# Optimization experiments

Hardware: AMD Instinct MI355X
Metric: run time of the kernel (lower is better)

The kernel has to match this reference:

```python
import jax, jax.numpy as jnp
import numpy as np
import math

B, S, D, H = 16, 1024, 768, 12
Dh = D // H  # 64


def setup_inputs() -> dict:
    key = jax.random.key(0)
    ks = jax.random.split(key, 9)
    scale = 1.0 / math.sqrt(D)
    X = jax.random.normal(ks[0], (B, S, D), dtype=jnp.float32)
    # Per-head Q/K/V projections stacked along head dim: [H, D, Dh]
    Wq = jax.random.normal(ks[1], (H, D, Dh), dtype=jnp.float32) * scale
    Wk = jax.random.normal(ks[2], (H, D, Dh), dtype=jnp.float32) * scale
    Wv = jax.random.normal(ks[3], (H, D, Dh), dtype=jnp.float32) * scale
    bq = jax.random.normal(ks[4], (H, Dh), dtype=jnp.float32) * scale
    bk = jax.random.normal(ks[5], (H, Dh), dtype=jnp.float32) * scale
    bv = jax.random.normal(ks[6], (H, Dh), dtype=jnp.float32) * scale
    Wo = jax.random.normal(ks[7], (D, D), dtype=jnp.float32) * scale
    bo = jax.random.normal(ks[8], (D,), dtype=jnp.float32) * scale
    return {"X": X, "Wq": Wq, "bq": bq, "Wk": Wk, "bk": bk,
            "Wv": Wv, "bv": bv, "Wo": Wo, "bo": bo}


def reference(X, Wq, bq, Wk, bk, Wv, bv, Wo, bo):
    # Batched multi-head QKV projections (equivalent to the per-head Linear loop).
    Q = jnp.einsum('bsd,hde->bhse', X, Wq) + bq[None, :, None, :]
    K = jnp.einsum('bsd,hde->bhse', X, Wk) + bk[None, :, None, :]
    V = jnp.einsum('bsd,hde->bhse', X, Wv) + bv[None, :, None, :]
    scores = jnp.einsum('bhse,bhte->bhst', Q, K) / jnp.sqrt(jnp.float32(Dh))
    A = jax.nn.softmax(scores, axis=-1)            # [B,H,S,S]
    O = jnp.einsum('bhst,bhte->bhse', A, V)        # [B,H,S,Dh]
    # Concat heads along feature dim (matches torch cat order: head 0 first).
    msa = jnp.transpose(O, (0, 2, 1, 3)).reshape(B, S, D)
    return msa @ Wo + bo
```

## Files before the change

### kernel.cpp

```cpp
#include <hip/hip_runtime.h>
#include <hip/hip_bf16.h>

#define BB 16
#define SS 1024
#define DD 768
#define HH 12
#define DH 64

typedef short short8 __attribute__((ext_vector_type(8)));
typedef float f32x4 __attribute__((ext_vector_type(4)));

__device__ inline float b2f(unsigned short v) {
    union { unsigned int u; float f; } x; x.u = ((unsigned int)v) << 16; return x.f;
}
__device__ inline unsigned short f2b(float f) {
    unsigned int u = __float_as_uint(f);
    u += 0x7FFFu + ((u >> 16) & 1u);
    return (unsigned short)(u >> 16);
}
__device__ inline unsigned int pk2(float a, float b) {
    __hip_bfloat162 h = __float22bfloat162_rn(make_float2(a, b));
    return *(unsigned int*)&h;
}
__device__ inline void cvt8(unsigned short* dst, const float* src) {
    const float4 f0 = *(const float4*)src;
    const float4 f1 = *(const float4*)(src + 4);
    unsigned short t[8] = {f2b(f0.x), f2b(f0.y), f2b(f0.z), f2b(f0.w),
                           f2b(f1.x), f2b(f1.y), f2b(f1.z), f2b(f1.w)};
    *(uint4*)dst = *(const uint4*)t;
}
__device__ __forceinline__ void async16(const void* g, void* l) {
    __builtin_amdgcn_global_load_lds(
        (const __attribute__((address_space(1))) void*)g,
        (__attribute__((address_space(3))) void*)l, 16, 0, 0);
}

__global__ __launch_bounds__(256) void detect_kernel(const unsigned short* __restrict__ X,
                                                     int* __restrict__ flag) {
    __shared__ int s;
    if (threadIdx.x == 0) s = 0;
    __syncthreads();
    int c = 0;
    for (int i = threadIdx.x; i < 16384; i += 256) {
        unsigned short v = X[i];
        if ((v & 0x7FFFu) >= 0x7F80u) c = 1;
    }
    if (c) s = 1;
    __syncthreads();
    if (threadIdx.x == 0) flag[0] = s;
}

__global__ __launch_bounds__(256) void prep_x(const void* __restrict__ Xv,
                                              const int* __restrict__ flag,
                                              unsigned short* __restrict__ Xb) {
    const int dt = *flag;
    size_t base = ((size_t)blockIdx.x * 256 + threadIdx.x) * 8;
    if (dt) cvt8(Xb + base, (const float*)Xv + base);
    else    *(uint4*)(Xb + base) = *(const uint4*)((const unsigned short*)Xv + base);
}

__global__ __launch_bounds__(256) void prep_w(
    const void* __restrict__ Wqv, const void* __restrict__ Wkv,
    const void* __restrict__ Wvv, const void* __restrict__ Wov,
    const int* __restrict__ flag,
    unsigned short* __restrict__ Wc, unsigned short* __restrict__ Wot)
{
    __shared__ unsigned short Ls[64][72];
    const int dt = *flag;
    const int u = threadIdx.x;
    const int kt = blockIdx.x;
    const int y  = blockIdx.y;
    const int rk = u >> 2;
    const int e0 = (u & 3) * 16;

    const void* src;
    size_t srcBase;
    unsigned short* dst; int drow;
    if (y < 36) {
        int z = y / 12, h = y % 12;
        src = (z == 0) ? Wqv : (z == 1) ? Wkv : Wvv;
        srcBase = ((size_t)h * DD + kt * 64 + rk) * DH;
        dst = Wc; drow = z * 768 + h * 64;
    } else {
        int nt = y - 36;
        src = Wov;
        srcBase = (size_t)(kt * 64 + rk) * DD + nt * 64;
        dst = Wot; drow = nt * 64;
    }

#pragma unroll
    for (int ii = 0; ii < 2; ++ii) {
        int e = e0 + ii * 8;
        if (dt) {
            const float* p = (const float*)src + srcBase + e;
            float4 a = *(const float4*)p, b = *(const float4*)(p + 4);
            float v[8] = {a.x, a.y, a.z, a.w, b.x, b.y, b.z, b.w};
#pragma unroll
            for (int j = 0; j < 8; ++j) Ls[e + j][rk] = f2b(v[j]);
        } else {
            union { uint4 v; unsigned short s[8]; } t;
            t.v = *(const uint4*)((const unsigned short*)src + srcBase + e);
#pragma unroll
            for (int j = 0; j < 8; ++j) Ls[e + j][rk] = t.s[j];
        }
    }
    __syncthreads();
    const int e = u >> 2, q = u & 3;
#pragma unroll
    for (int ii = 0; ii < 2; ++ii) {
        int kk = q * 16 + ii * 8;
        *(uint4*)(dst + (size_t)(drow + e) * DD + kt * 64 + kk) = *(const uint4*)(&Ls[e][kk]);
    }
}

__global__ __launch_bounds__(256) void prep_bias(
    const void* __restrict__ bqv, const void* __restrict__ bkv,
    const void* __restrict__ bvv, const void* __restrict__ bov,
    const int* __restrict__ flag,
    unsigned short* __restrict__ bc, float* __restrict__ bo32)
{
    const int dt = *flag;
    for (int n = threadIdx.x; n < 2304; n += 256) {
        int z = n / 768, i = n % 768;
        const void* b = (z == 0) ? bqv : (z == 1) ? bkv : bvv;
        bc[n] = dt ? f2b(((const float*)b)[i]) : ((const unsigned short*)b)[i];
    }
    for (int n = threadIdx.x; n < 768; n += 256)
        bo32[n] = dt ? ((const float*)bov)[n] : b2f(((const unsigned short*)bov)[n]);
}

__global__ __launch_bounds__(256) void qkv_gemm(
    const unsigned short* __restrict__ Xb,
    const unsigned short* __restrict__ Wc,
    const unsigned short* __restrict__ bc,
    unsigned short* __restrict__ Qb, unsigned short* __restrict__ Kb,
    unsigned short* __restrict__ Vtb)
{
    __shared__ __align__(16) unsigned short lds[17408];
    unsigned short* As = lds;
    unsigned short* Bs = lds + 128 * 64;

    const int u = threadIdx.x;
    const int lane = u & 63, w = u >> 6;
    const int ln = lane & 15, quad = lane >> 4;
    const int wm = w & 1, wn = w >> 1;

    const int nt0 = blockIdx.x;
    const int m0  = blockIdx.y << 7;
    const int n0  = nt0 << 7;
    const int z   = nt0 / 6;
    const int hpair = (nt0 % 6) * 2;

    const int rA = w * 32 + (lane >> 3);
    const int c8 = (((lane & 7) ^ (lane >> 3)) * 8);

    f32x4 acc[4][4];
#pragma unroll
    for (int i = 0; i < 4; ++i)
#pragma unroll
        for (int j = 0; j < 4; ++j) acc[i][j] = (f32x4){0.f, 0.f, 0.f, 0.f};

    const unsigned short* Ag = Xb + (size_t)(m0 + rA) * DD + c8;
    const unsigned short* Bg = Wc + (size_t)(n0 + rA) * DD + c8;
    unsigned short* lA0 = As + w * 2048;
    unsigned short* lB0 = Bs + w * 2048;

    for (int kb = 0; kb < 12; ++kb) {
        const int k0 = kb * 64;
        if (kb) __syncthreads();
#pragma unroll
        for (int j = 0; j < 4; ++j) {
            async16(Ag + (size_t)j * 8 * DD + k0, lA0 + j * 512);
            async16(Bg + (size_t)j * 8 * DD + k0, lB0 + j * 512);
        }
        __syncthreads();
#pragma unroll
        for (int kh = 0; kh < 2; ++kh) {
            const int sx = ((kh * 4 + quad) ^ (ln & 7)) * 8;
            short8 af[4], bf[4];
#pragma unroll
            for (int t = 0; t < 4; ++t) {
                af[t] = *(const short8*)(As + (wm * 64 + t * 16 + ln) * 64 + sx);
                bf[t] = *(const short8*)(Bs + (wn * 64 + t * 16 + ln) * 64 + sx);
            }
#pragma unroll
            for (int mt = 0; mt < 4; ++mt)
#pragma unroll
                for (int nt = 0; nt < 4; ++nt)
                    acc[mt][nt] = __builtin_amdgcn_mfma_f32_16x16x32_bf16(af[mt], bf[nt], acc[mt][nt], 0, 0, 0);
        }
    }

    float bias[4];
#pragma unroll
    for (int nt = 0; nt < 4; ++nt) bias[nt] = b2f(bc[n0 + wn * 64 + nt * 16 + ln]);

    const int b = m0 >> 10;
    if (z < 2) {
        unsigned short* O = (z == 0) ? Qb : Kb;
        const int h = hpair + wn;
        const int sb = (m0 & 1023) + wm * 64;
#pragma unroll
        for (int mt = 0; mt < 4; ++mt)
#pragma unroll
            for (int r = 0; r < 4; ++r) {
                int s = sb + mt * 16 + quad * 4 + r;
                size_t rowo = ((size_t)(b * HH + h) * SS + s) * DH;
#pragma unroll
                for (int nt = 0; nt < 4; ++nt)
                    O[rowo + nt * 16 + ln] = f2b(acc[mt][nt][r] + bias[nt]);
            }
    } else {
        __syncthreads();
#pragma unroll
        for (int mt = 0; mt < 4; ++mt)
#pragma unroll
            for (int nt = 0; nt < 4; ++nt)
#pragma unroll
                for (int r = 0; r < 4; ++r)
                    lds[(wn * 64 + nt * 16 + ln) * 136 + wm * 64 + mt * 16 + quad * 4 + r] =
                        f2b(acc[mt][nt][r] + bias[nt]);
        __syncthreads();
        const int cc = u >> 1, half = u & 1;
        const int h = hpair + (cc >> 6), e = cc & 63;
        const int sb = (m0 & 1023) + half * 64;
        unsigned short* dst = Vtb + ((size_t)(b * HH + h) * DH + e) * SS + sb;
        const unsigned short* srcp = lds + cc * 136 + half * 64;
#pragma unroll
        for (int i = 0; i < 8; ++i)
            *(uint4*)(dst + i * 8) = *(const uint4*)(srcp + i * 8);
    }
}

__global__ __launch_bounds__(256) void attn_kernel(
    const unsigned short* __restrict__ Kb,
    const unsigned short* __restrict__ Vtb,
    unsigned short* __restrict__ Qb)
{
    __shared__ __align__(16) unsigned short Qs[64][72];
    __shared__ __align__(16) unsigned short Ks[4096];
    __shared__ __align__(16) unsigned short Vs[4096];
    __shared__ __align__(16) unsigned short Ps[64][72];

    const int u = threadIdx.x;
    const int s0 = blockIdx.x << 6;
    const int bh = blockIdx.y;

    const int lane = u & 63, w = u >> 6;
    const int ln = lane & 15, quad = lane >> 4;

    unsigned short* Qg = Qb + ((size_t)bh * SS + s0) * DH;
    const unsigned short* Kg = Kb + (size_t)bh * SS * DH;
    const unsigned short* Vg = Vtb + (size_t)bh * DH * SS;

    const int xrow = u >> 3, xch = u & 7;
#pragma unroll
    for (int p = 0; p < 2; ++p) {
        int r2 = xrow + 32 * p;
        *(uint4*)(&Qs[r2][xch * 8]) = *(const uint4*)(Qg + r2 * DH + xch * 8);
    }
    __syncthreads();
    short8 qf0 = *(const short8*)(&Qs[16 * w + ln][quad * 8]);
    short8 qf1 = *(const short8*)(&Qs[16 * w + ln][32 + quad * 8]);

    short8 ones;
#pragma unroll
    for (int i = 0; i < 8; ++i) ones[i] = (short)0x3F80;

    f32x4 acc_o[4];
#pragma unroll
    for (int i = 0; i < 4; ++i) acc_o[i] = (f32x4){0.f, 0.f, 0.f, 0.f};
    f32x4 acc_l = (f32x4){0.f, 0.f, 0.f, 0.f};

    const float Csc = 0.125f * 1.44269504088896f;

    const int srow = (lane >> 3);
    const int cg8  = ((lane & 7) ^ srow) * 8;

    for (int kt = 0; kt < 16; ++kt) {
        const int t0 = kt << 6;
        __syncthreads();
#pragma unroll
        for (int j = 0; j < 2; ++j) {
            const int r0 = (w * 2 + j) * 8 + srow;
            async16(Kg + (size_t)(t0 + r0) * DH + cg8, Ks + (w * 2 + j) * 512);
            async16(Vg + (size_t)r0 * SS + t0 + cg8,  Vs + (w * 2 + j) * 512);
        }
        __syncthreads();

        f32x4 acc_s[4];
#pragma unroll
        for (int nt = 0; nt < 4; ++nt) {
            const int sx0 = (quad ^ (ln & 7)) * 8;
            const int sx1 = ((4 + quad) ^ (ln & 7)) * 8;
            short8 kf0 = *(const short8*)(Ks + (nt * 16 + ln) * 64 + sx0);
            short8 kf1 = *(const short8*)(Ks + (nt * 16 + ln) * 64 + sx1);
            f32x4 zz = (f32x4){0.f, 0.f, 0.f, 0.f};
            zz = __builtin_amdgcn_mfma_f32_16x16x32_bf16(kf0, qf0, zz, 0, 0, 0);
            zz = __builtin_amdgcn_mfma_f32_16x16x32_bf16(kf1, qf1, zz, 0, 0, 0);
            acc_s[nt] = zz;
        }

#pragma unroll
        for (int nt = 0; nt < 4; ++nt) {
            float p0 = exp2f(acc_s[nt][0] * Csc);
            float p1 = exp2f(acc_s[nt][1] * Csc);
            float p2 = exp2f(acc_s[nt][2] * Csc);
            float p3 = exp2f(acc_s[nt][3] * Csc);
            uint2 pw;
            pw.x = pk2(p0, p1);
            pw.y = pk2(p2, p3);
            *(uint2*)(&Ps[16 * w + ln][nt * 16 + quad * 4]) = pw;
        }

        short8 pf0 = *(const short8*)(&Ps[16 * w + ln][quad * 8]);
        short8 pf1 = *(const short8*)(&Ps[16 * w + ln][32 + quad * 8]);
        acc_l = __builtin_amdgcn_mfma_f32_16x16x32_bf16(pf0, ones, acc_l, 0, 0, 0);
        acc_l = __builtin_amdgcn_mfma_f32_16x16x32_bf16(pf1, ones, acc_l, 0, 0, 0);
#pragma unroll
        for (int nt = 0; nt < 4; ++nt) {
            const int sx0 = (quad ^ (ln & 7)) * 8;
            const int sx1 = ((4 + quad) ^ (ln & 7)) * 8;
            short8 vf0 = *(const short8*)(Vs + (nt * 16 + ln) * 64 + sx0);
            short8 vf1 = *(const short8*)(Vs + (nt * 16 + ln) * 64 + sx1);
            acc_o[nt] = __builtin_amdgcn_mfma_f32_16x16x32_bf16(pf0, vf0, acc_o[nt], 0, 0, 0);
            acc_o[nt] = __builtin_amdgcn_mfma_f32_16x16x32_bf16(pf1, vf1, acc_o[nt], 0, 0, 0);
        }
    }

    float inv[4];
#pragma unroll
    for (int r = 0; r < 4; ++r) inv[r] = 1.f / acc_l[r];
#pragma unroll
    for (int nt = 0; nt < 4; ++nt)
#pragma unroll
        for (int r = 0; r < 4; ++r) {
            int row = 16 * w + quad * 4 + r;
            Qg[row * DH + nt * 16 + ln] = f2b(acc_o[nt][r] * inv[r]);
        }
}

__global__ __launch_bounds__(256) void oproj_gemm(
    const unsigned short* __restrict__ Ob,
    const unsigned short* __restrict__ Wot,
    const float* __restrict__ bo32,
    float* __restrict__ out)
{
    __shared__ __align__(16) unsigned short lds[128 * 128];
    unsigned short* As = lds;
    unsigned short* Bs = lds + 128 * 64;

    const int u = threadIdx.x;
    const int lane = u & 63, w = u >> 6;
    const int ln = lane & 15, quad = lane >> 4;
    const int wm = w & 1, wn = w >> 1;

    const int n0 = blockIdx.x << 7;
    const int m0 = blockIdx.y << 7;
    const int b = m0 >> 10, s0t = m0 & 1023;

    const int rA = w * 32 + (lane >> 3);
    const int c8 = (((lane & 7) ^ (lane >> 3)) * 8);

    f32x4 acc[4][4];
#pragma unroll
    for (int i = 0; i < 4; ++i)
#pragma unroll
        for (int j = 0; j < 4; ++j) acc[i][j] = (f32x4){0.f, 0.f, 0.f, 0.f};

    const unsigned short* Bg = Wot + (size_t)(n0 + rA) * DD + c8;
    unsigned short* lA0 = As + w * 2048;
    unsigned short* lB0 = Bs + w * 2048;

    for (int kb = 0; kb < 12; ++kb) {
        if (kb) __syncthreads();
        const unsigned short* Ag = Ob + ((size_t)(b * HH + kb) * SS + s0t + rA) * DH + c8;
#pragma unroll
        for (int j = 0; j < 4; ++j) {
            async16(Ag + (size_t)j * 8 * DH, lA0 + j * 512);
            async16(Bg + (size_t)j * 8 * DD + kb * 64, lB0 + j * 512);
        }
        __syncthreads();
#pragma unroll
        for (int kh = 0; kh < 2; ++kh) {
            const int sx = ((kh * 4 + quad) ^ (ln & 7)) * 8;
            short8 af[4], bf[4];
#pragma unroll
            for (int t = 0; t < 4; ++t) {
                af[t] = *(const short8*)(As + (wm * 64 + t * 16 + ln) * 64 + sx);
                bf[t] = *(const short8*)(Bs + (wn * 64 + t * 16 + ln) * 64 + sx);
            }
#pragma unroll
            for (int mt = 0; mt < 4; ++mt)
#pragma unroll
                for (int nt = 0; nt < 4; ++nt)
                    acc[mt][nt] = __builtin_amdgcn_mfma_f32_16x16x32_bf16(af[mt], bf[nt], acc[mt][nt], 0, 0, 0);
        }
    }

    float bias[4];
#pragma unroll
    for (int nt = 0; nt < 4; ++nt) bias[nt] = bo32[n0 + wn * 64 + nt * 16 + ln];
#pragma unroll
    for (int mt = 0; mt < 4; ++mt)
#pragma unroll
        for (int r = 0; r < 4; ++r) {
            int m = m0 + wm * 64 + mt * 16 + quad * 4 + r;
            float* orow = out + (size_t)m * DD + n0 + wn * 64;
#pragma unroll
            for (int nt = 0; nt < 4; ++nt)
                orow[nt * 16 + ln] = acc[mt][nt][r] + bias[nt];
        }
}

extern "C" void kernel_launch(void* const* d_in, const int* in_sizes, int n_in,
                              void* d_out, int out_size, void* d_ws, size_t ws_size,
                              hipStream_t stream)
{
    const void* X  = d_in[0];
    const void* Wq = d_in[1];
    const void* bq = d_in[2];
    const void* Wk = d_in[3];
    const void* bk = d_in[4];
    const void* Wv = d_in[5];
    const void* bv = d_in[6];
    const void* Wo = d_in[7];
    const void* bo = d_in[8];
    float* out = (float*)d_out;

    const size_t NE = (size_t)BB * HH * SS * DH;
    char* p = (char*)d_ws;
    int* flag = (int*)p;                 p += 256;
    unsigned short* Qb  = (unsigned short*)p;  p += NE * 2;
    unsigned short* Kb  = (unsigned short*)p;  p += NE * 2;
    unsigned short* Vtb = (unsigned short*)p;  p += NE * 2;
    unsigned short* Xb  = (unsigned short*)p;  p += (size_t)BB * SS * DD * 2;
    unsigned short* Wc  = (unsigned short*)p;  p += (size_t)3 * DD * DD * 2;
    unsigned short* Wot = (unsigned short*)p;  p += (size_t)DD * DD * 2;
    unsigned short* bcb = (unsigned short*)p;  p += 4608;
    float* bo32 = (float*)p;                   p += 3072;

    detect_kernel<<<1, 256, 0, stream>>>((const unsigned short*)X, flag);
    prep_x<<<6144, 256, 0, stream>>>(X, flag, Xb);
    prep_w<<<dim3(12, 48), 256, 0, stream>>>(Wq, Wk, Wv, Wo, flag, Wc, Wot);
    prep_bias<<<1, 256, 0, stream>>>(bq, bk, bv, bo, flag, bcb, bo32);
    qkv_gemm<<<dim3(18, 128), 256, 0, stream>>>(Xb, Wc, bcb, Qb, Kb, Vtb);
    attn_kernel<<<dim3(16, 192), 256, 0, stream>>>(Kb, Vtb, Qb);
    oproj_gemm<<<dim3(6, 128), 256, 0, stream>>>(Qb, Wot, bo32, out);
}
```

Measured before the change: 337.1 us.

## Merge prep kernels, fold softmax scale into Q, slim attention LDS and addressing

Three preprocessing kernels (X conversion, weight transpose, bias) are merged into one launch to cut launch overhead. The softmax scale times log2(e) is folded into the Q projection epilogue, which removes a multiply per score in the attention inner loop. The attention kernel reuses the Q LDS buffer for P, adds a launch-bounds occupancy hint, and precomputes pointer and swizzle addresses outside the loop. Rounding Q to bf16 after scaling slightly changes precision, and softmax still runs without a max subtraction.

```diff
diff --git a/kernel.cpp b/kernel.cpp
--- a/kernel.cpp
+++ b/kernel.cpp
@@ -50,82 +50,79 @@
     if (threadIdx.x == 0) flag[0] = s;
 }
 
-__global__ __launch_bounds__(256) void prep_x(const void* __restrict__ Xv,
-                                              const int* __restrict__ flag,
-                                              unsigned short* __restrict__ Xb) {
-    const int dt = *flag;
-    size_t base = ((size_t)blockIdx.x * 256 + threadIdx.x) * 8;
-    if (dt) cvt8(Xb + base, (const float*)Xv + base);
-    else    *(uint4*)(Xb + base) = *(const uint4*)((const unsigned short*)Xv + base);
-}
-
-__global__ __launch_bounds__(256) void prep_w(
-    const void* __restrict__ Wqv, const void* __restrict__ Wkv,
-    const void* __restrict__ Wvv, const void* __restrict__ Wov,
+__global__ __launch_bounds__(256) void prep_all(
+    const void* __restrict__ Xv,
+    const void* __restrict__ Wqv, const void* __restrict__ bqv,
+    const void* __restrict__ Wkv, const void* __restrict__ bkv,
+    const void* __restrict__ Wvv, const void* __restrict__ bvv,
+    const void* __restrict__ Wov, const void* __restrict__ bov,
     const int* __restrict__ flag,
-    unsigned short* __restrict__ Wc, unsigned short* __restrict__ Wot)
+    unsigned short* __restrict__ Xb, unsigned short* __restrict__ Wc,
+    unsigned short* __restrict__ Wot, unsigned short* __restrict__ bc,
+    float* __restrict__ bo32)
 {
     __shared__ unsigned short Ls[64][72];
     const int dt = *flag;
     const int u = threadIdx.x;
-    const int kt = blockIdx.x;
-    const int y  = blockIdx.y;
-    const int rk = u >> 2;
-    const int e0 = (u & 3) * 16;
-
-    const void* src;
-    size_t srcBase;
-    unsigned short* dst; int drow;
-    if (y < 36) {
-        int z = y / 12, h = y % 12;
-        src = (z == 0) ? Wqv : (z == 1) ? Wkv : Wvv;
-        srcBase = ((size_t)h * DD + kt * 64 + rk) * DH;
-        dst = Wc; drow = z * 768 + h * 64;
-    } else {
-        int nt = y - 36;
-        src = Wov;
-        srcBase = (size_t)(kt * 64 + rk) * DD + nt * 64;
-        dst = Wot; drow = nt * 64;
-    }
-
-#pragma unroll
-    for (int ii = 0; ii < 2; ++ii) {
-        int e = e0 + ii * 8;
-        if (dt) {
-            const float* p = (const float*)src + srcBase + e;
-            float4 a = *(const float4*)p, b = *(const float4*)(p + 4);
-            float v[8] = {a.x, a.y, a.z, a.w, b.x, b.y, b.z, b.w};
-#pragma unroll
-            for (int j = 0; j < 8; ++j) Ls[e + j][rk] = f2b(v[j]);
+    const int bx = blockIdx.x;
+
+    if (bx < 6144) {
+        size_t base = ((size_t)bx * 256 + u) * 8;
+        if (dt) cvt8(Xb + base, (const float*)Xv + base);
+        else    *(uint4*)(Xb + base) = *(const uint4*)((const unsigned short*)Xv + base);
+        return;
+    }
+    if (bx < 6720) {
+        const int idx = bx - 6144;
+        const int kt = idx % 12;
+        const int y  = idx / 12;
+        const int rk = u >> 2;
+        const int e0 = (u & 3) * 16;
+
+        const void* src; size_t srcBase;
+        unsigned short* dst; int drow;
+        if (y < 36) {
+            int z = y / 12, h = y % 12;
+            src = (z == 0) ? Wqv : (z == 1) ? Wkv : Wvv;
+            srcBase = ((size_t)h * DD + kt * 64 + rk) * DH;
+            dst = Wc; drow = z * 768 + h * 64;
         } else {
-            union { uint4 v; unsigned short s[8]; } t;
-            t.v = *(const uint4*)((const unsigned short*)src + srcBase + e);
-#pragma unroll
-            for (int j = 0; j < 8; ++j) Ls[e + j][rk] = t.s[j];
-        }
-    }
-    __syncthreads();
-    const int e = u >> 2, q = u & 3;
-#pragma unroll
-    for (int ii = 0; ii < 2; ++ii) {
-        int kk = q * 16 + ii * 8;
-        *(uint4*)(dst + (size_t)(drow + e) * DD + kt * 64 + kk) = *(const uint4*)(&Ls[e][kk]);
-    }
-}
-
-__global__ __launch_bounds__(256) void prep_bias(
-    const void* __restrict__ bqv, const void* __restrict__ bkv,
-    const void* __restrict__ bvv, const void* __restrict__ bov,
-    const int* __restrict__ flag,
-    unsigned short* __restrict__ bc, float* __restrict__ bo32)
-{
-    const int dt = *flag;
-    for (int n = threadIdx.x; n < 2304; n += 256) {
+            int nt = y - 36;
+            src = Wov;
+            srcBase = (size_t)(kt * 64 + rk) * DD + nt * 64;
+            dst = Wot; drow = nt * 64;
+        }
+#pragma unroll
+        for (int ii = 0; ii < 2; ++ii) {
+            int e = e0 + ii * 8;
+            if (dt) {
+                const float* p = (const float*)src + srcBase + e;
+                float4 a = *(const float4*)p, b = *(const float4*)(p + 4);
+                float v[8] = {a.x, a.y, a.z, a.w, b.x, b.y, b.z, b.w};
+#pragma unroll
+                for (int j = 0; j < 8; ++j) Ls[e + j][rk] = f2b(v[j]);
+            } else {
+                union { uint4 v; unsigned short s[8]; } t;
+                t.v = *(const uint4*)((const unsigned short*)src + srcBase + e);
+#pragma unroll
+                for (int j = 0; j < 8; ++j) Ls[e + j][rk] = t.s[j];
+            }
+        }
+        __syncthreads();
+        const int e = u >> 2, q = u & 3;
+#pragma unroll
+        for (int ii = 0; ii < 2; ++ii) {
+            int kk = q * 16 + ii * 8;
+            *(uint4*)(dst + (size_t)(drow + e) * DD + kt * 64 + kk) = *(const uint4*)(&Ls[e][kk]);
+        }
+        return;
+    }
+    for (int n = u; n < 2304; n += 256) {
         int z = n / 768, i = n % 768;
         const void* b = (z == 0) ? bqv : (z == 1) ? bkv : bvv;
         bc[n] = dt ? f2b(((const float*)b)[i]) : ((const unsigned short*)b)[i];
     }
-    for (int n = threadIdx.x; n < 768; n += 256)
+    for (int n = u; n < 768; n += 256)
         bo32[n] = dt ? ((const float*)bov)[n] : b2f(((const unsigned short*)bov)[n]);
 }
 
@@ -198,6 +195,7 @@
     const int b = m0 >> 10;
     if (z < 2) {
         unsigned short* O = (z == 0) ? Qb : Kb;
+        const float sc = (z == 0) ? 0.180336880111120f : 1.0f;
         const int h = hpair + wn;
         const int sb = (m0 & 1023) + wm * 64;
 #pragma unroll
@@ -208,7 +206,7 @@
                 size_t rowo = ((size_t)(b * HH + h) * SS + s) * DH;
 #pragma unroll
                 for (int nt = 0; nt < 4; ++nt)
-                    O[rowo + nt * 16 + ln] = f2b(acc[mt][nt][r] + bias[nt]);
+                    O[rowo + nt * 16 + ln] = f2b((acc[mt][nt][r] + bias[nt]) * sc);
             }
     } else {
         __syncthreads();
@@ -232,15 +230,14 @@
     }
 }
 
-__global__ __launch_bounds__(256) void attn_kernel(
+__global__ __launch_bounds__(256, 6) void attn_kernel(
     const unsigned short* __restrict__ Kb,
     const unsigned short* __restrict__ Vtb,
     unsigned short* __restrict__ Qb)
 {
-    __shared__ __align__(16) unsigned short Qs[64][72];
+    __shared__ __align__(16) unsigned short QPs[64][72];
     __shared__ __align__(16) unsigned short Ks[4096];
     __shared__ __align__(16) unsigned short Vs[4096];
-    __shared__ __align__(16) unsigned short Ps[64][72];
 
     const int u = threadIdx.x;
     const int s0 = blockIdx.x << 6;
@@ -257,11 +254,11 @@
 #pragma unroll
     for (int p = 0; p < 2; ++p) {
         int r2 = xrow + 32 * p;
-        *(uint4*)(&Qs[r2][xch * 8]) = *(const uint4*)(Qg + r2 * DH + xch * 8);
+        *(uint4*)(&QPs[r2][xch * 8]) = *(const uint4*)(Qg + r2 * DH + xch * 8);
     }
     __syncthreads();
-    short8 qf0 = *(const short8*)(&Qs[16 * w + ln][quad * 8]);
-    short8 qf1 = *(const short8*)(&Qs[16 * w + ln][32 + quad * 8]);
+    short8 qf0 = *(const short8*)(&QPs[16 * w + ln][quad * 8]);
+    short8 qf1 = *(const short8*)(&QPs[16 * w + ln][32 + quad * 8]);
 
     short8 ones;
 #pragma unroll
@@ -272,29 +269,37 @@
     for (int i = 0; i < 4; ++i) acc_o[i] = (f32x4){0.f, 0.f, 0.f, 0.f};
     f32x4 acc_l = (f32x4){0.f, 0.f, 0.f, 0.f};
 
-    const float Csc = 0.125f * 1.44269504088896f;
-
-    const int srow = (lane >> 3);
+    const int srow = lane >> 3;
     const int cg8  = ((lane & 7) ^ srow) * 8;
+    const unsigned short* kp0 = Kg + (size_t)((w * 2 + 0) * 8 + srow) * DH + cg8;
+    const unsigned short* kp1 = Kg + (size_t)((w * 2 + 1) * 8 + srow) * DH + cg8;
+    const unsigned short* vp0 = Vg + (size_t)((w * 2 + 0) * 8 + srow) * SS + cg8;
+    const unsigned short* vp1 = Vg + (size_t)((w * 2 + 1) * 8 + srow) * SS + cg8;
+    unsigned short* lk0 = Ks + (w * 2 + 0) * 512;
+    unsigned short* lk1 = Ks + (w * 2 + 1) * 512;
+    unsigned short* lv0 = Vs + (w * 2 + 0) * 512;
+    unsigned short* lv1 = Vs + (w * 2 + 1) * 512;
+
+    const unsigned short* kb0 = Ks + ln * 64 + ((quad) ^ (ln & 7)) * 8;
+    const unsigned short* kb1 = Ks + ln * 64 + ((4 + quad) ^ (ln & 7)) * 8;
+    const unsigned short* vb0 = Vs + ln * 64 + ((quad) ^ (ln & 7)) * 8;
+    const unsigned short* vb1 = Vs + ln * 64 + ((4 + quad) ^ (ln & 7)) * 8;
+    unsigned short* psw = &QPs[16 * w + ln][quad * 4];
+    const unsigned short* psr0 = &QPs[16 * w + ln][quad * 8];
+    const unsigned short* psr1 = &QPs[16 * w + ln][32 + quad * 8];
 
     for (int kt = 0; kt < 16; ++kt) {
-        const int t0 = kt << 6;
-        __syncthreads();
-#pragma unroll
-        for (int j = 0; j < 2; ++j) {
-            const int r0 = (w * 2 + j) * 8 + srow;
-            async16(Kg + (size_t)(t0 + r0) * DH + cg8, Ks + (w * 2 + j) * 512);
-            async16(Vg + (size_t)r0 * SS + t0 + cg8,  Vs + (w * 2 + j) * 512);
-        }
+        __syncthreads();
+        async16(kp0, lk0); async16(kp1, lk1);
+        async16(vp0, lv0); async16(vp1, lv1);
+        kp0 += 64 * DH; kp1 += 64 * DH; vp0 += 64; vp1 += 64;
         __syncthreads();
 
         f32x4 acc_s[4];
 #pragma unroll
         for (int nt = 0; nt < 4; ++nt) {
-            const int sx0 = (quad ^ (ln & 7)) * 8;
-            const int sx1 = ((4 + quad) ^ (ln & 7)) * 8;
-            short8 kf0 = *(const short8*)(Ks + (nt * 16 + ln) * 64 + sx0);
-            short8 kf1 = *(const short8*)(Ks + (nt * 16 + ln) * 64 + sx1);
+            short8 kf0 = *(const short8*)(kb0 + nt * 1024);
+            short8 kf1 = *(const short8*)(kb1 + nt * 1024);
             f32x4 zz = (f32x4){0.f, 0.f, 0.f, 0.f};
             zz = __builtin_amdgcn_mfma_f32_16x16x32_bf16(kf0, qf0, zz, 0, 0, 0);
             zz = __builtin_amdgcn_mfma_f32_16x16x32_bf16(kf1, qf1, zz, 0, 0, 0);
@@ -303,26 +308,20 @@
 
 #pragma unroll
         for (int nt = 0; nt < 4; ++nt) {
-            float p0 = exp2f(acc_s[nt][0] * Csc);
-            float p1 = exp2f(acc_s[nt][1] * Csc);
-            float p2 = exp2f(acc_s[nt][2] * Csc);
-            float p3 = exp2f(acc_s[nt][3] * Csc);
             uint2 pw;
-            pw.x = pk2(p0, p1);
-            pw.y = pk2(p2, p3);
-            *(uint2*)(&Ps[16 * w + ln][nt * 16 + quad * 4]) = pw;
-        }
-
-        short8 pf0 = *(const short8*)(&Ps[16 * w + ln][quad * 8]);
-        short8 pf1 = *(const short8*)(&Ps[16 * w + ln][32 + quad * 8]);
+            pw.x = pk2(exp2f(acc_s[nt][0]), exp2f(acc_s[nt][1]));
+            pw.y = pk2(exp2f(acc_s[nt][2]), exp2f(acc_s[nt][3]));
+            *(uint2*)(psw + nt * 16) = pw;
+        }
+
+        short8 pf0 = *(const short8*)psr0;
+        short8 pf1 = *(const short8*)psr1;
         acc_l = __builtin_amdgcn_mfma_f32_16x16x32_bf16(pf0, ones, acc_l, 0, 0, 0);
         acc_l = __builtin_amdgcn_mfma_f32_16x16x32_bf16(pf1, ones, acc_l, 0, 0, 0);
 #pragma unroll
         for (int nt = 0; nt < 4; ++nt) {
-            const int sx0 = (quad ^ (ln & 7)) * 8;
-            const int sx1 = ((4 + quad) ^ (ln & 7)) * 8;
-            short8 vf0 = *(const short8*)(Vs + (nt * 16 + ln) * 64 + sx0);
-            short8 vf1 = *(const short8*)(Vs + (nt * 16 + ln) * 64 + sx1);
+            short8 vf0 = *(const short8*)(vb0 + nt * 1024);
+            short8 vf1 = *(const short8*)(vb1 + nt * 1024);
             acc_o[nt] = __builtin_amdgcn_mfma_f32_16x16x32_bf16(pf0, vf0, acc_o[nt], 0, 0, 0);
             acc_o[nt] = __builtin_amdgcn_mfma_f32_16x16x32_bf16(pf1, vf1, acc_o[nt], 0, 0, 0);
         }
@@ -441,9 +440,8 @@
     float* bo32 = (float*)p;                   p += 3072;
 
     detect_kernel<<<1, 256, 0, stream>>>((const unsigned short*)X, flag);
-    prep_x<<<6144, 256, 0, stream>>>(X, flag, Xb);
-    prep_w<<<dim3(12, 48), 256, 0, stream>>>(Wq, Wk, Wv, Wo, flag, Wc, Wot);
-    prep_bias<<<1, 256, 0, stream>>>(bq, bk, bv, bo, flag, bcb, bo32);
+    prep_all<<<6721, 256, 0, stream>>>(X, Wq, bq, Wk, bk, Wv, bv, Wo, bo, flag,
+                                       Xb, Wc, Wot, bcb, bo32);
     qkv_gemm<<<dim3(18, 128), 256, 0, stream>>>(Xb, Wc, bcb, Qb, Kb, Vtb);
     attn_kernel<<<dim3(16, 192), 256, 0, stream>>>(Kb, Vtb, Qb);
     oproj_gemm<<<dim3(6, 128), 256, 0, stream>>>(Qb, Wot, bo32, out);
```

After: 326.2 us. 3.2% less time.
